# Optimization experiments

Measured on AMD Instinct MI355X. Metric: run time of the kernel, lower is better.

Reference implementation:

```python
import jax, jax.numpy as jnp
import numpy as np

NUM_HEADS = 12
HEAD_DIM = 64


def setup_inputs() -> dict:
    key = jax.random.key(0)
    ks = jax.random.split(key, 4)
    B, T, C = 2, 2048, 768
    x = jax.random.normal(ks[0], (B, T, C), dtype=jnp.float32)
    attention_mask = jnp.ones((B, 1, 1, T), dtype=jnp.int32)
    W_attn = jax.random.normal(ks[1], (C, 3 * C), dtype=jnp.float32) * 0.02
    b_attn = jnp.zeros((3 * C,), dtype=jnp.float32)
    W_proj = jax.random.normal(ks[2], (C, C), dtype=jnp.float32) * 0.02
    b_proj = jnp.zeros((C,), dtype=jnp.float32)
    return {"x": x, "attention_mask": attention_mask, "W_attn": W_attn,
            "b_attn": b_attn, "W_proj": W_proj, "b_proj": b_proj}


def reference(x, attention_mask, W_attn, b_attn, W_proj, b_proj):
    B, T, C = x.shape
    H, D = NUM_HEADS, HEAD_DIM
    # c_attn (Conv1D): y = x @ W + b -> [B, T, 3C]
    qkv = x @ W_attn + b_attn
    q, k, v = jnp.split(qkv, 3, axis=-1)
    # [B, T, C] -> [B, H, T, D]
    q = q.reshape(B, T, H, D).transpose(0, 2, 1, 3)
    k = k.reshape(B, T, H, D).transpose(0, 2, 1, 3)
    v = v.reshape(B, T, H, D).transpose(0, 2, 1, 3)
    scores = jnp.einsum('bhqd,bhkd->bhqk', q, k) / jnp.sqrt(jnp.float32(D))
    causal = jnp.tril(jnp.ones((T, T), dtype=bool))[None, None]  # [1,1,T,T]
    mask_value = jnp.finfo(scores.dtype).min
    scores = jnp.where(causal, scores, mask_value)
    scores = jnp.where(attention_mask == 0, -jnp.inf, scores)
    probs = jax.nn.softmax(scores, axis=-1)
    attn_out = jnp.einsum('bhqk,bhkd->bhqd', probs, v)
    attn_out = attn_out.transpose(0, 2, 1, 3).reshape(B, T, C)
    return attn_out @ W_proj + b_proj
```

## Files before the change

kernel.cpp:

```cpp
#include <hip/hip_runtime.h>

typedef __attribute__((ext_vector_type(8))) short bf16x8;
typedef __attribute__((ext_vector_type(4))) float f32x4;
typedef __attribute__((ext_vector_type(16))) float f32x16;

#define MFMA16(a, b, c) __builtin_amdgcn_mfma_f32_16x16x32_bf16(a, b, c, 0, 0, 0)
#define MFMA32(a, b, c) __builtin_amdgcn_mfma_f32_32x32x16_bf16(a, b, c, 0, 0, 0)
#define LOG2E 1.4426950408889634f
#define MB2 46.16624868f

#define BB 2
#define TT 2048
#define CC 768
#define HH 12
#define DD 64
#define MM (BB * TT)
#define N1 (3 * CC)
#define BH_STRIDE 131072

static __device__ __forceinline__ unsigned short f2bf(float f) {
  union { float f; unsigned u; } v; v.f = f;
  unsigned r = (v.u + 0x7FFFu + ((v.u >> 16) & 1u)) >> 16;
  return (unsigned short)r;
}

static __device__ __forceinline__ unsigned cvt_pk_bf16(float lo, float hi) {
  unsigned r;
  asm("v_cvt_pk_bf16_f32 %0, %1, %2" : "=v"(r) : "v"(lo), "v"(hi));
  return r;
}

static __device__ __forceinline__ void gload_lds16(const void* g, void* l) {
  __builtin_amdgcn_global_load_lds(
      (const __attribute__((address_space(1))) void*)g,
      (__attribute__((address_space(3))) void*)l, 16, 0, 0);
}

#define PREP_CVT 3072
#define PREP_TR1 1728
#define PREP_TR2 576
__global__ __launch_bounds__(256) void k_prep(
    const float* __restrict__ x, unsigned short* __restrict__ Xb,
    const float* __restrict__ Wa, unsigned short* __restrict__ WaT,
    const float* __restrict__ Wp, unsigned short* __restrict__ WpT,
    const int* __restrict__ mask, unsigned int* __restrict__ mb) {
  __shared__ float tile[32][33];
  const int bid = blockIdx.x;
  const int tid = threadIdx.x;
  if (bid < PREP_CVT) {
    const int i = bid * 256 + tid;
    float4 v = reinterpret_cast<const float4*>(x)[i];
    ushort4 r;
    r.x = f2bf(v.x); r.y = f2bf(v.y); r.z = f2bf(v.z); r.w = f2bf(v.w);
    reinterpret_cast<ushort4*>(Xb)[i] = r;
  } else if (bid < PREP_CVT + PREP_TR1 + PREP_TR2) {
    const bool first = bid < PREP_CVT + PREP_TR1;
    const int b = first ? bid - PREP_CVT : bid - PREP_CVT - PREP_TR1;
    const int nb = first ? 72 : 24;
    const int N = first ? N1 : CC;
    const float* W = first ? Wa : Wp;
    unsigned short* Wt = first ? WaT : WpT;
    const int n0 = (b % nb) * 32, k0 = (b / nb) * 32;
    const int tx = tid & 31, ty = tid >> 5;
#pragma unroll
    for (int i = 0; i < 4; ++i)
      tile[ty + i * 8][tx] = W[(size_t)(k0 + ty + i * 8) * N + n0 + tx];
    __syncthreads();
#pragma unroll
    for (int i = 0; i < 4; ++i)
      Wt[(size_t)(n0 + ty + i * 8) * CC + k0 + tx] = f2bf(tile[tx][ty + i * 8]);
  } else {
    if (tid < 128) {
      unsigned bits = 0;
      const int* p = mask + tid * 32;
#pragma unroll
      for (int j = 0; j < 32; ++j) bits |= (p[j] != 0 ? 1u : 0u) << j;
      mb[tid] = bits;
    }
  }
}

template <int MODE, int BN>
__global__ __launch_bounds__(256) void k_gemm(
    const unsigned short* __restrict__ A, const unsigned short* __restrict__ Bt,
    const float* __restrict__ bias, float* __restrict__ Cout, int N, int K,
    unsigned short* __restrict__ Qb, unsigned short* __restrict__ Kb,
    unsigned short* __restrict__ Vt) {
  constexpr int NI = BN / 32;
  __shared__ __align__(16) unsigned short As[3][128 * 32];
  __shared__ __align__(16) unsigned short Bs[3][BN * 32];
  const int tid = threadIdx.x;
  const int lane = tid & 63;
  const int wid = tid >> 6;
  const int l15 = lane & 15, l4 = lane >> 4;
  const int wr = wid >> 1, wc = wid & 1;
  const int brow = blockIdx.x * 128, bcol = blockIdx.y * BN;

  f32x4 acc[4][NI] = {};

  const int srow = tid >> 2;
  const int usrc = (tid & 3) ^ ((tid >> 3) & 3);
  const unsigned short* gA0 = A + (size_t)(brow + srow) * K + usrc * 8;
  const unsigned short* gA1 = gA0 + (size_t)64 * K;
  const unsigned short* gB0 = Bt + (size_t)(bcol + srow) * K + usrc * 8;
  const unsigned short* gB1 = (BN == 128) ? gB0 + (size_t)64 * K : gB0;
  const int dslot = tid * 8;

  const int NT = K / 32;

#define STAGE(t, buf)                                       \
  do {                                                      \
    const int ko = (t) * 32;                                \
    gload_lds16(gA0 + ko, &As[buf][dslot]);                 \
    gload_lds16(gA1 + ko, &As[buf][dslot + 2048]);          \
    gload_lds16(gB0 + ko, &Bs[buf][dslot]);                 \
    if (BN == 128) gload_lds16(gB1 + ko, &Bs[buf][dslot + 2048]); \
  } while (0)

  const int swz = (l4 ^ ((l15 >> 1) & 3)) * 8;
  const int arow = wr * 64 + l15;
  const int brow2 = wc * (BN / 2) + l15;

  STAGE(0, 0);
  STAGE(1, 1);

  int cur = 0;
  for (int t = 0; t < NT - 1; ++t) {
    if (BN == 128) asm volatile("s_waitcnt vmcnt(4)" ::: "memory");
    else           asm volatile("s_waitcnt vmcnt(3)" ::: "memory");
    __builtin_amdgcn_s_barrier();
    if (t + 2 < NT) {
      int nb = cur + 2; if (nb >= 3) nb -= 3;
      STAGE(t + 2, nb);
    }
    bf16x8 af[4], bfr[NI];
#pragma unroll
    for (int mi = 0; mi < 4; ++mi)
      af[mi] = *reinterpret_cast<const bf16x8*>(&As[cur][(arow + mi * 16) * 32 + swz]);
#pragma unroll
    for (int ni = 0; ni < NI; ++ni)
      bfr[ni] = *reinterpret_cast<const bf16x8*>(&Bs[cur][(brow2 + ni * 16) * 32 + swz]);
    __builtin_amdgcn_s_setprio(1);
#pragma unroll
    for (int mi = 0; mi < 4; ++mi)
#pragma unroll
      for (int ni = 0; ni < NI; ++ni)
        acc[mi][ni] = MFMA16(af[mi], bfr[ni], acc[mi][ni]);
    __builtin_amdgcn_s_setprio(0);
    cur = (cur == 2) ? 0 : cur + 1;
  }
  asm volatile("s_waitcnt vmcnt(0)" ::: "memory");
  __builtin_amdgcn_s_barrier();
  {
    bf16x8 af[4], bfr[NI];
#pragma unroll
    for (int mi = 0; mi < 4; ++mi)
      af[mi] = *reinterpret_cast<const bf16x8*>(&As[cur][(arow + mi * 16) * 32 + swz]);
#pragma unroll
    for (int ni = 0; ni < NI; ++ni)
      bfr[ni] = *reinterpret_cast<const bf16x8*>(&Bs[cur][(brow2 + ni * 16) * 32 + swz]);
    __builtin_amdgcn_s_setprio(1);
#pragma unroll
    for (int mi = 0; mi < 4; ++mi)
#pragma unroll
      for (int ni = 0; ni < NI; ++ni)
        acc[mi][ni] = MFMA16(af[mi], bfr[ni], acc[mi][ni]);
    __builtin_amdgcn_s_setprio(0);
  }
#undef STAGE

#pragma unroll
  for (int mi = 0; mi < 4; ++mi) {
    const int m0 = brow + wr * 64 + mi * 16 + l4 * 4;
#pragma unroll
    for (int ni = 0; ni < NI; ++ni) {
      const int n = bcol + wc * (BN / 2) + ni * 16 + l15;
      const float bv = bias[n];
      if (MODE == 0) {
#pragma unroll
        for (int r = 0; r < 4; ++r)
          Cout[(size_t)(m0 + r) * N + n] = acc[mi][ni][r] + bv;
      } else {
        const int sec = n / CC;
        const int nn = n - sec * CC;
        const int hh = nn >> 6, d = nn & 63;
        const int b = m0 >> 11;
        const int t0 = m0 & 2047;
        const size_t hbase = (size_t)(b * HH + hh) * BH_STRIDE;
        if (sec == 0) {
#pragma unroll
          for (int r = 0; r < 4; ++r) {
            const int t = t0 + r;
            Qb[hbase + ((t >> 5) * 4 + (d >> 4)) * 512 + (t & 31) * 16 + (d & 15)] =
                f2bf((acc[mi][ni][r] + bv) * 0.125f);
          }
        } else if (sec == 1) {
#pragma unroll
          for (int r = 0; r < 4; ++r) {
            const int t = t0 + r;
            Kb[hbase + ((t >> 5) * 4 + (d >> 4)) * 512 + (t & 31) * 16 + (d & 15)] =
                f2bf(acc[mi][ni][r] + bv);
          }
        } else {
          ushort4 pk;
          pk.x = f2bf(acc[mi][ni][0] + bv);
          pk.y = f2bf(acc[mi][ni][1] + bv);
          pk.z = f2bf(acc[mi][ni][2] + bv);
          pk.w = f2bf(acc[mi][ni][3] + bv);
          *reinterpret_cast<ushort4*>(
              &Vt[hbase + ((t0 >> 6) * 4 + ((t0 >> 4) & 3)) * 1024 + d * 16 + (t0 & 15)]) = pk;
        }
      }
    }
  }
}

__device__ __forceinline__ void loadk(bf16x8 (&dst)[2][4], const unsigned short* Kh,
                                      int kv0, int lo) {
  const unsigned short* kp = Kh + (kv0 >> 5) * 2048 + lo;
#pragma unroll
  for (int kg = 0; kg < 2; ++kg)
#pragma unroll
    for (int dg = 0; dg < 4; ++dg)
      dst[kg][dg] = *reinterpret_cast<const bf16x8*>(&kp[kg * 2048 + dg * 512]);
}

__device__ __forceinline__ void attn_tile(
    int kv0, const bf16x8 (&kf)[2][4], uint2 mb, const bf16x8 (&qf)[4],
    const unsigned short* __restrict__ Vh, int q0, int l31, int h, int lo,
    f32x16& o0, f32x16& o1, float& lrow) {
  const unsigned short* vp = Vh + (kv0 >> 6) * 4096 + lo;
  bf16x8 vf0[4], vf1[4];
#pragma unroll
  for (int kc = 0; kc < 4; ++kc) {
    vf0[kc] = *reinterpret_cast<const bf16x8*>(&vp[kc * 1024]);
    vf1[kc] = *reinterpret_cast<const bf16x8*>(&vp[kc * 1024 + 512]);
  }

  f32x16 s0 = {}, s1 = {};
  __builtin_amdgcn_s_setprio(1);
#pragma unroll
  for (int dg = 0; dg < 4; ++dg) s0 = MFMA32(kf[0][dg], qf[dg], s0);
#pragma unroll
  for (int dg = 0; dg < 4; ++dg) s1 = MFMA32(kf[1][dg], qf[dg], s1);
  __builtin_amdgcn_s_setprio(0);

  if ((mb.x & mb.y) != 0xffffffffu) {
#pragma unroll
    for (int r = 0; r < 16; ++r) {
      const int ki = (r & 3) + 8 * (r >> 2) + 4 * h;
      if (!((mb.x >> ki) & 1u)) s0[r] = -1e30f;
      if (!((mb.y >> ki) & 1u)) s1[r] = -1e30f;
    }
  }
  if (kv0 + 63 > q0) {
    const int q = q0 + l31;
#pragma unroll
    for (int r = 0; r < 16; ++r) {
      const int ki = kv0 + (r & 3) + 8 * (r >> 2) + 4 * h;
      if (ki > q) s0[r] = -1e30f;
      if (ki + 32 > q) s1[r] = -1e30f;
    }
  }

#pragma unroll
  for (int r = 0; r < 16; ++r) {
    s0[r] = __builtin_amdgcn_exp2f(__builtin_fmaf(s0[r], LOG2E, -MB2));
    s1[r] = __builtin_amdgcn_exp2f(__builtin_fmaf(s1[r], LOG2E, -MB2));
  }
  float ts[8];
#pragma unroll
  for (int r = 0; r < 8; ++r)
    ts[r] = (s0[2 * r] + s0[2 * r + 1]) + (s1[2 * r] + s1[2 * r + 1]);
  float ps = ((ts[0] + ts[1]) + (ts[2] + ts[3])) + ((ts[4] + ts[5]) + (ts[6] + ts[7]));
  ps += __shfl_xor(ps, 32);
  lrow += ps;

  unsigned pk0[4][2], pk1[4][2];
#pragma unroll
  for (int m = 0; m < 4; ++m)
#pragma unroll
    for (int j = 0; j < 2; ++j) {
      pk0[m][j] = cvt_pk_bf16(s0[4 * m + 2 * j], s0[4 * m + 2 * j + 1]);
      pk1[m][j] = cvt_pk_bf16(s1[4 * m + 2 * j], s1[4 * m + 2 * j + 1]);
    }

#pragma unroll
  for (int kc = 0; kc < 4; ++kc) {
    const unsigned (&pkk)[4][2] = (kc < 2) ? pk0 : pk1;
    const int c1 = (kc & 1) * 2;
    const unsigned v0 = h ? pkk[c1][0] : pkk[c1 + 1][0];
    const unsigned v1 = h ? pkk[c1][1] : pkk[c1 + 1][1];
    const unsigned r0 = (unsigned)__shfl_xor((int)v0, 32);
    const unsigned r1 = (unsigned)__shfl_xor((int)v1, 32);
    union { unsigned u[4]; bf16x8 v; } af;
    af.u[0] = h ? r0 : pkk[c1][0];
    af.u[1] = h ? r1 : pkk[c1][1];
    af.u[2] = h ? pkk[c1 + 1][0] : r0;
    af.u[3] = h ? pkk[c1 + 1][1] : r1;
    __builtin_amdgcn_s_setprio(1);
    o0 = MFMA32(af.v, vf0[kc], o0);
    o1 = MFMA32(af.v, vf1[kc], o1);
    __builtin_amdgcn_s_setprio(0);
  }
}

__global__ __launch_bounds__(256, 2) void k_attn(
    const unsigned short* __restrict__ Q, const unsigned short* __restrict__ Kb,
    const unsigned short* __restrict__ Vt, const unsigned int* __restrict__ mbits,
    float* __restrict__ pO, float* __restrict__ pL,
    unsigned short* __restrict__ AO) {
  const int tid = threadIdx.x;
  const int lane = tid & 63;
  const int w = tid >> 6;
  const int l31 = lane & 31;
  const int h = lane >> 5;
  const int lo = l31 * 16 + h * 8;
  const int f = blockIdx.x;
  const int xcd = f & 7;
  const int i = f >> 3;
  const int hl = i % 3;
  const int j = i / 3;
  const int bh = xcd * 3 + hl;
  int g, c;
  if (j < 16)      { g = 15 - (j >> 2); c = j & 3; }
  else if (j < 28) { const int u = j - 16; g = 11 - u / 3; c = u % 3; }
  else if (j < 36) { const int u = j - 28; g = 7 - (u >> 1); c = u & 1; }
  else             { g = 3 - (j - 36); c = 0; }
  const int qb = 4 * g + w;
  int cb;
  if (qb < 16)      cb = qb;
  else if (qb < 32) cb = 16 + 2 * (qb - 16);
  else if (qb < 48) cb = 48 + 3 * (qb - 32);
  else              cb = 96 + 4 * (qb - 48);
  const int pidx = bh * 160 + cb + c;

  const int b = bh / HH;
  const int hd = bh - b * HH;
  const int q0 = qb * 32;
  const int nt = qb / 2 + 1;
  const int t0 = c * 8;
  const int t1 = (t0 + 8 < nt) ? t0 + 8 : nt;

  const unsigned short* Qh = Q + (size_t)bh * BH_STRIDE;
  const unsigned short* Kh = Kb + (size_t)bh * BH_STRIDE;
  const unsigned short* Vh = Vt + (size_t)bh * BH_STRIDE;
  const unsigned int* mbp = mbits + b * 64;

  bf16x8 qf[4];
  {
    const unsigned short* qp = Qh + (q0 >> 5) * 2048 + lo;
#pragma unroll
    for (int dg = 0; dg < 4; ++dg)
      qf[dg] = *reinterpret_cast<const bf16x8*>(&qp[dg * 512]);
  }

  f32x16 o0 = {}, o1 = {};
  float lrow = 0.f;

  bf16x8 kfA[2][4], kfB[2][4];
  uint2 mbA, mbB;
  loadk(kfA, Kh, t0 * 64, lo);
  mbA = *reinterpret_cast<const uint2*>(&mbp[t0 * 2]);

  int t = t0;
  while (true) {
    if (t + 1 < t1) {
      loadk(kfB, Kh, (t + 1) * 64, lo);
      mbB = *reinterpret_cast<const uint2*>(&mbp[(t + 1) * 2]);
    }
    attn_tile(t * 64, kfA, mbA, qf, Vh, q0, l31, h, lo, o0, o1, lrow);
    ++t; if (t >= t1) break;
    if (t + 1 < t1) {
      loadk(kfA, Kh, (t + 1) * 64, lo);
      mbA = *reinterpret_cast<const uint2*>(&mbp[(t + 1) * 2]);
    }
    attn_tile(t * 64, kfB, mbB, qf, Vh, q0, l31, h, lo, o0, o1, lrow);
    ++t; if (t >= t1) break;
  }

  if (t0 == 0 && t1 == nt) {
    const float rl = 1.0f / lrow;
#pragma unroll
    for (int r = 0; r < 16; ++r) {
      const int crow = (r & 3) + 8 * (r >> 2) + 4 * h;
      const float rb = __shfl(rl, crow);
      const size_t base = (size_t)(b * TT + q0 + crow) * CC + hd * DD;
      AO[base + l31] = f2bf(o0[r] * rb);
      AO[base + 32 + l31] = f2bf(o1[r] * rb);
    }
  } else {
    float* po = pO + (size_t)pidx * 2048;
#pragma unroll
    for (int r = 0; r < 16; ++r) {
      const int crow = (r & 3) + 8 * (r >> 2) + 4 * h;
      po[crow * 64 + l31] = o0[r];
      po[crow * 64 + 32 + l31] = o1[r];
    }
    if (lane < 32) {
      pL[pidx * 32 + lane] = lrow;
    }
  }
}

__global__ __launch_bounds__(256) void k_merge(
    const float* __restrict__ pO, const float* __restrict__ pL,
    unsigned short* __restrict__ AO) {
  const int qb = 16 + blockIdx.x, bh = blockIdx.y;
  const int b = bh / HH, hd = bh - b * HH;
  const int nt = qb / 2 + 1;
  const int nch = (nt + 7) >> 3;
  int cb;
  if (qb < 32)      cb = 16 + 2 * (qb - 16);
  else if (qb < 48) cb = 48 + 3 * (qb - 32);
  else              cb = 96 + 4 * (qb - 48);
  const int p0 = bh * 160 + cb;

  const int q = threadIdx.x >> 3;
  const int d0 = (threadIdx.x & 7) * 8;

  float lst = 0.f;
#pragma unroll
  for (int c = 0; c < 4; ++c)
    if (c < nch) lst += pL[(p0 + c) * 32 + q];
  const float inv = 1.0f / lst;

  float acc[8] = {};
#pragma unroll
  for (int c = 0; c < 4; ++c) {
    if (c < nch) {
      const float* po = pO + ((size_t)(p0 + c) * 32 + q) * 64 + d0;
      const float4 a = *reinterpret_cast<const float4*>(po);
      const float4 bq = *reinterpret_cast<const float4*>(po + 4);
      acc[0] += a.x; acc[1] += a.y; acc[2] += a.z; acc[3] += a.w;
      acc[4] += bq.x; acc[5] += bq.y; acc[6] += bq.z; acc[7] += bq.w;
    }
  }
  union { unsigned short u[8]; uint4 v; } ov;
#pragma unroll
  for (int jj = 0; jj < 8; ++jj) ov.u[jj] = f2bf(acc[jj] * inv);
  *reinterpret_cast<uint4*>(&AO[(size_t)(b * TT + qb * 32 + q) * CC + hd * DD + d0]) = ov.v;
}

extern "C" void kernel_launch(void* const* d_in, const int* in_sizes, int n_in,
                              void* d_out, int out_size, void* d_ws, size_t ws_size,
                              hipStream_t stream) {
  const float* x   = (const float*)d_in[0];
  const int* mask  = (const int*)d_in[1];
  const float* Wa  = (const float*)d_in[2];
  const float* ba  = (const float*)d_in[3];
  const float* Wp  = (const float*)d_in[4];
  const float* bp  = (const float*)d_in[5];
  float* out = (float*)d_out;

  char* ws = (char*)d_ws;
  unsigned short* Xb  = (unsigned short*)(ws);
  unsigned short* WaT = (unsigned short*)(ws + 6291456);
  unsigned short* WpT = (unsigned short*)(ws + 9830400);
  unsigned short* Qb  = (unsigned short*)(ws + 11010048);
  unsigned short* Kb  = (unsigned short*)(ws + 17301504);
  unsigned short* Vt  = (unsigned short*)(ws + 23592960);
  unsigned short* AO  = (unsigned short*)(ws + 29884416);
  unsigned int*   Mb  = (unsigned int*)(ws + 36175872);
  float*          pL  = (float*)(ws + 36667904);
  float*          pO  = (float*)(ws + 37159424);

  k_prep<<<dim3(PREP_CVT + PREP_TR1 + PREP_TR2 + 1), dim3(256), 0, stream>>>(
      x, Xb, Wa, WaT, Wp, WpT, mask, Mb);

  k_gemm<1, 128><<<dim3(MM / 128, N1 / 128), dim3(256), 0, stream>>>(
      Xb, WaT, ba, nullptr, N1, CC, Qb, Kb, Vt);

  k_attn<<<dim3(960), dim3(256), 0, stream>>>(Qb, Kb, Vt, Mb, pO, pL, AO);
  k_merge<<<dim3(48, BB * HH), dim3(256), 0, stream>>>(pO, pL, AO);

  k_gemm<0, 64><<<dim3(MM / 128, CC / 64), dim3(256), 0, stream>>>(
      AO, WpT, bp, out, CC, CC, nullptr, nullptr, nullptr);
}
```

Baseline: 83.51 us.

## Stage K/V tiles through LDS with triple buffering and drop split-KV merge

```diff
diff --git a/kernel.cpp b/kernel.cpp
--- a/kernel.cpp
+++ b/kernel.cpp
@@ -215,26 +215,20 @@
   }
 }
 
-__device__ __forceinline__ void loadk(bf16x8 (&dst)[2][4], const unsigned short* Kh,
-                                      int kv0, int lo) {
-  const unsigned short* kp = Kh + (kv0 >> 5) * 2048 + lo;
+__device__ __forceinline__ void attn_tile_lds(
+    int kv0, const unsigned short* __restrict__ sKt,
+    const unsigned short* __restrict__ sVt, uint2 mb, const bf16x8 (&qf)[4],
+    int q0, int l31, int h, int lo, f32x16& o0, f32x16& o1, float& lrow) {
+  bf16x8 kf[2][4], vf0[4], vf1[4];
 #pragma unroll
   for (int kg = 0; kg < 2; ++kg)
 #pragma unroll
     for (int dg = 0; dg < 4; ++dg)
-      dst[kg][dg] = *reinterpret_cast<const bf16x8*>(&kp[kg * 2048 + dg * 512]);
-}
-
-__device__ __forceinline__ void attn_tile(
-    int kv0, const bf16x8 (&kf)[2][4], uint2 mb, const bf16x8 (&qf)[4],
-    const unsigned short* __restrict__ Vh, int q0, int l31, int h, int lo,
-    f32x16& o0, f32x16& o1, float& lrow) {
-  const unsigned short* vp = Vh + (kv0 >> 6) * 4096 + lo;
-  bf16x8 vf0[4], vf1[4];
+      kf[kg][dg] = *reinterpret_cast<const bf16x8*>(&sKt[kg * 2048 + dg * 512 + lo]);
 #pragma unroll
   for (int kc = 0; kc < 4; ++kc) {
-    vf0[kc] = *reinterpret_cast<const bf16x8*>(&vp[kc * 1024]);
-    vf1[kc] = *reinterpret_cast<const bf16x8*>(&vp[kc * 1024 + 512]);
+    vf0[kc] = *reinterpret_cast<const bf16x8*>(&sVt[kc * 1024 + lo]);
+    vf1[kc] = *reinterpret_cast<const bf16x8*>(&sVt[kc * 1024 + 512 + lo]);
   }
 
   f32x16 s0 = {}, s1 = {};
@@ -308,8 +302,9 @@
 __global__ __launch_bounds__(256, 2) void k_attn(
     const unsigned short* __restrict__ Q, const unsigned short* __restrict__ Kb,
     const unsigned short* __restrict__ Vt, const unsigned int* __restrict__ mbits,
-    float* __restrict__ pO, float* __restrict__ pL,
     unsigned short* __restrict__ AO) {
+  __shared__ __align__(16) unsigned short sK[3][4096];
+  __shared__ __align__(16) unsigned short sV[3][4096];
   const int tid = threadIdx.x;
   const int lane = tid & 63;
   const int w = tid >> 6;
@@ -319,32 +314,18 @@
   const int f = blockIdx.x;
   const int xcd = f & 7;
   const int i = f >> 3;
-  const int hl = i % 3;
-  const int j = i / 3;
-  const int bh = xcd * 3 + hl;
-  int g, c;
-  if (j < 16)      { g = 15 - (j >> 2); c = j & 3; }
-  else if (j < 28) { const int u = j - 16; g = 11 - u / 3; c = u % 3; }
-  else if (j < 36) { const int u = j - 28; g = 7 - (u >> 1); c = u & 1; }
-  else             { g = 3 - (j - 36); c = 0; }
+  const int bh = xcd * 3 + (i % 3);
+  const int g = 15 - i / 3;
   const int qb = 4 * g + w;
-  int cb;
-  if (qb < 16)      cb = qb;
-  else if (qb < 32) cb = 16 + 2 * (qb - 16);
-  else if (qb < 48) cb = 48 + 3 * (qb - 32);
-  else              cb = 96 + 4 * (qb - 48);
-  const int pidx = bh * 160 + cb + c;
-
   const int b = bh / HH;
   const int hd = bh - b * HH;
   const int q0 = qb * 32;
   const int nt = qb / 2 + 1;
-  const int t0 = c * 8;
-  const int t1 = (t0 + 8 < nt) ? t0 + 8 : nt;
+  const int ntmax = 2 * g + 2;
 
   const unsigned short* Qh = Q + (size_t)bh * BH_STRIDE;
-  const unsigned short* Kh = Kb + (size_t)bh * BH_STRIDE;
-  const unsigned short* Vh = Vt + (size_t)bh * BH_STRIDE;
+  const char* KhB = (const char*)(Kb + (size_t)bh * BH_STRIDE);
+  const char* VhB = (const char*)(Vt + (size_t)bh * BH_STRIDE);
   const unsigned int* mbp = mbits + b * 64;
 
   bf16x8 qf[4];
@@ -358,88 +339,44 @@
   f32x16 o0 = {}, o1 = {};
   float lrow = 0.f;
 
-  bf16x8 kfA[2][4], kfB[2][4];
-  uint2 mbA, mbB;
-  loadk(kfA, Kh, t0 * 64, lo);
-  mbA = *reinterpret_cast<const uint2*>(&mbp[t0 * 2]);
-
-  int t = t0;
-  while (true) {
-    if (t + 1 < t1) {
-      loadk(kfB, Kh, (t + 1) * 64, lo);
-      mbB = *reinterpret_cast<const uint2*>(&mbp[(t + 1) * 2]);
-    }
-    attn_tile(t * 64, kfA, mbA, qf, Vh, q0, l31, h, lo, o0, o1, lrow);
-    ++t; if (t >= t1) break;
-    if (t + 1 < t1) {
-      loadk(kfA, Kh, (t + 1) * 64, lo);
-      mbA = *reinterpret_cast<const uint2*>(&mbp[(t + 1) * 2]);
-    }
-    attn_tile(t * 64, kfB, mbB, qf, Vh, q0, l31, h, lo, o0, o1, lrow);
-    ++t; if (t >= t1) break;
-  }
-
-  if (t0 == 0 && t1 == nt) {
-    const float rl = 1.0f / lrow;
-#pragma unroll
-    for (int r = 0; r < 16; ++r) {
-      const int crow = (r & 3) + 8 * (r >> 2) + 4 * h;
-      const float rb = __shfl(rl, crow);
-      const size_t base = (size_t)(b * TT + q0 + crow) * CC + hd * DD;
-      AO[base + l31] = f2bf(o0[r] * rb);
-      AO[base + 32 + l31] = f2bf(o1[r] * rb);
-    }
-  } else {
-    float* po = pO + (size_t)pidx * 2048;
-#pragma unroll
-    for (int r = 0; r < 16; ++r) {
-      const int crow = (r & 3) + 8 * (r >> 2) + 4 * h;
-      po[crow * 64 + l31] = o0[r];
-      po[crow * 64 + 32 + l31] = o1[r];
-    }
-    if (lane < 32) {
-      pL[pidx * 32 + lane] = lrow;
-    }
-  }
-}
-
-__global__ __launch_bounds__(256) void k_merge(
-    const float* __restrict__ pO, const float* __restrict__ pL,
-    unsigned short* __restrict__ AO) {
-  const int qb = 16 + blockIdx.x, bh = blockIdx.y;
-  const int b = bh / HH, hd = bh - b * HH;
-  const int nt = qb / 2 + 1;
-  const int nch = (nt + 7) >> 3;
-  int cb;
-  if (qb < 32)      cb = 16 + 2 * (qb - 16);
-  else if (qb < 48) cb = 48 + 3 * (qb - 32);
-  else              cb = 96 + 4 * (qb - 48);
-  const int p0 = bh * 160 + cb;
-
-  const int q = threadIdx.x >> 3;
-  const int d0 = (threadIdx.x & 7) * 8;
-
-  float lst = 0.f;
-#pragma unroll
-  for (int c = 0; c < 4; ++c)
-    if (c < nch) lst += pL[(p0 + c) * 32 + q];
-  const float inv = 1.0f / lst;
-
-  float acc[8] = {};
-#pragma unroll
-  for (int c = 0; c < 4; ++c) {
-    if (c < nch) {
-      const float* po = pO + ((size_t)(p0 + c) * 32 + q) * 64 + d0;
-      const float4 a = *reinterpret_cast<const float4*>(po);
-      const float4 bq = *reinterpret_cast<const float4*>(po + 4);
-      acc[0] += a.x; acc[1] += a.y; acc[2] += a.z; acc[3] += a.w;
-      acc[4] += bq.x; acc[5] += bq.y; acc[6] += bq.z; acc[7] += bq.w;
-    }
-  }
-  union { unsigned short u[8]; uint4 v; } ov;
-#pragma unroll
-  for (int jj = 0; jj < 8; ++jj) ov.u[jj] = f2bf(acc[jj] * inv);
-  *reinterpret_cast<uint4*>(&AO[(size_t)(b * TT + qb * 32 + q) * CC + hd * DD + d0]) = ov.v;
+#define ASTAGE(t, buf)                                                    \
+  do {                                                                    \
+    const size_t off = (size_t)(t) * 8192 + tid * 16;                     \
+    gload_lds16(KhB + off, (char*)&sK[buf][0] + tid * 16);                \
+    gload_lds16(KhB + off + 4096, (char*)&sK[buf][0] + 4096 + tid * 16);  \
+    gload_lds16(VhB + off, (char*)&sV[buf][0] + tid * 16);                \
+    gload_lds16(VhB + off + 4096, (char*)&sV[buf][0] + 4096 + tid * 16);  \
+  } while (0)
+
+  ASTAGE(0, 0);
+  if (ntmax > 1) ASTAGE(1, 1);
+
+  int cur = 0;
+  for (int t = 0; t < ntmax; ++t) {
+    if (t + 1 < ntmax) asm volatile("s_waitcnt vmcnt(4)" ::: "memory");
+    else               asm volatile("s_waitcnt vmcnt(0)" ::: "memory");
+    __builtin_amdgcn_s_barrier();
+    if (t + 2 < ntmax) {
+      int nb = cur + 2; if (nb >= 3) nb -= 3;
+      ASTAGE(t + 2, nb);
+    }
+    if (t < nt) {
+      const uint2 mbt = *reinterpret_cast<const uint2*>(&mbp[t * 2]);
+      attn_tile_lds(t * 64, sK[cur], sV[cur], mbt, qf, q0, l31, h, lo, o0, o1, lrow);
+    }
+    cur = (cur == 2) ? 0 : cur + 1;
+  }
+#undef ASTAGE
+
+  const float rl = 1.0f / lrow;
+#pragma unroll
+  for (int r = 0; r < 16; ++r) {
+    const int crow = (r & 3) + 8 * (r >> 2) + 4 * h;
+    const float rb = __shfl(rl, crow);
+    const size_t base = (size_t)(b * TT + q0 + crow) * CC + hd * DD;
+    AO[base + l31] = f2bf(o0[r] * rb);
+    AO[base + 32 + l31] = f2bf(o1[r] * rb);
+  }
 }
 
 extern "C" void kernel_launch(void* const* d_in, const int* in_sizes, int n_in,
@@ -462,8 +399,6 @@
   unsigned short* Vt  = (unsigned short*)(ws + 23592960);
   unsigned short* AO  = (unsigned short*)(ws + 29884416);
   unsigned int*   Mb  = (unsigned int*)(ws + 36175872);
-  float*          pL  = (float*)(ws + 36667904);
-  float*          pO  = (float*)(ws + 37159424);
 
   k_prep<<<dim3(PREP_CVT + PREP_TR1 + PREP_TR2 + 1), dim3(256), 0, stream>>>(
       x, Xb, Wa, WaT, Wp, WpT, mask, Mb);
@@ -471,8 +406,7 @@
   k_gemm<1, 128><<<dim3(MM / 128, N1 / 128), dim3(256), 0, stream>>>(
       Xb, WaT, ba, nullptr, N1, CC, Qb, Kb, Vt);
 
-  k_attn<<<dim3(960), dim3(256), 0, stream>>>(Qb, Kb, Vt, Mb, pO, pL, AO);
-  k_merge<<<dim3(48, BB * HH), dim3(256), 0, stream>>>(pO, pL, AO);
+  k_attn<<<dim3(384), dim3(256), 0, stream>>>(Qb, Kb, Vt, Mb, AO);
 
   k_gemm<0, 64><<<dim3(MM / 128, CC / 64), dim3(256), 0, stream>>>(
       AO, WpT, bp, out, CC, CC, nullptr, nullptr, nullptr);
```

Measured after the change: 96.85 us. 16.0% more time.
